# Kernel optimization log

Hardware: AMD Instinct MI355X
Metric: run time of the kernel (lower is better)

The kernel has to match this reference:

```python
import jax, jax.numpy as jnp
import numpy as np
import math

HIDDEN = 2048
N_HEADS = 32
N_KV_HEADS = 8
HEAD_DIM = HIDDEN // N_HEADS  # 64
N_REP = N_HEADS // N_KV_HEADS  # 4
ROPE_THETA = 10000.0
BSZ, SEQ = 2, 2048


def setup_inputs() -> dict:
    key = jax.random.key(0)
    ks = jax.random.split(key, 6)
    hidden_states = jax.random.normal(ks[0], (BSZ, SEQ, HIDDEN), dtype=jnp.float32)
    wq = jax.random.normal(ks[1], (HIDDEN, N_HEADS * HEAD_DIM), dtype=jnp.float32) * (HIDDEN ** -0.5)
    wk = jax.random.normal(ks[2], (HIDDEN, N_KV_HEADS * HEAD_DIM), dtype=jnp.float32) * (HIDDEN ** -0.5)
    wv = jax.random.normal(ks[3], (HIDDEN, N_KV_HEADS * HEAD_DIM), dtype=jnp.float32) * (HIDDEN ** -0.5)
    wo = jax.random.normal(ks[4], (N_HEADS * HEAD_DIM, HIDDEN), dtype=jnp.float32) * (HIDDEN ** -0.5)
    # additive causal mask [b, 1, q, kv]
    neg = jnp.finfo(jnp.float32).min
    causal = jnp.where(jnp.tril(jnp.ones((SEQ, SEQ), dtype=bool)), 0.0, neg)
    attention_mask = jnp.broadcast_to(causal[None, None], (BSZ, 1, SEQ, SEQ)).astype(jnp.float32)
    position_ids = jnp.broadcast_to(jnp.arange(SEQ, dtype=jnp.int32)[None], (BSZ, SEQ))
    return {
        "hidden_states": hidden_states,
        "wq": wq, "wk": wk, "wv": wv, "wo": wo,
        "attention_mask": attention_mask,
        "position_ids": position_ids,
    }


def _rope_cache(seq_len, dtype):
    inv_freq = 1.0 / (ROPE_THETA ** (jnp.arange(0, HEAD_DIM, 2, dtype=jnp.float32) / HEAD_DIM))
    t = jnp.arange(seq_len, dtype=jnp.float32)
    freqs = jnp.outer(t, inv_freq)              # [S, head_dim/2]
    emb = jnp.concatenate([freqs, freqs], -1)   # [S, head_dim]
    return jnp.cos(emb).astype(dtype), jnp.sin(emb).astype(dtype)


def _rotate_half(x):
    x1, x2 = jnp.split(x, 2, axis=-1)
    return jnp.concatenate([-x2, x1], axis=-1)


def reference(hidden_states, wq, wk, wv, wo, attention_mask, position_ids):
    b, s, _ = hidden_states.shape
    q = (hidden_states @ wq).reshape(b, s, N_HEADS, HEAD_DIM).transpose(0, 2, 1, 3)
    k = (hidden_states @ wk).reshape(b, s, N_KV_HEADS, HEAD_DIM).transpose(0, 2, 1, 3)
    v = (hidden_states @ wv).reshape(b, s, N_KV_HEADS, HEAD_DIM).transpose(0, 2, 1, 3)

    cos_c, sin_c = _rope_cache(s, hidden_states.dtype)
    cos = cos_c[position_ids][:, None]  # [b,1,s,head_dim]
    sin = sin_c[position_ids][:, None]
    q = q * cos + _rotate_half(q) * sin
    k = k * cos + _rotate_half(k) * sin

    # repeat_kv: [b, kvh, s, d] -> [b, kvh*n_rep, s, d]
    k = jnp.broadcast_to(k[:, :, None], (b, N_KV_HEADS, N_REP, s, HEAD_DIM)).reshape(b, N_HEADS, s, HEAD_DIM)
    v = jnp.broadcast_to(v[:, :, None], (b, N_KV_HEADS, N_REP, s, HEAD_DIM)).reshape(b, N_HEADS, s, HEAD_DIM)

    scores = jnp.einsum('bhqd,bhkd->bhqk', q, k) / math.sqrt(HEAD_DIM)
    scores = scores + attention_mask
    probs = jax.nn.softmax(scores.astype(jnp.float32), axis=-1).astype(q.dtype)
    attn = jnp.einsum('bhqk,bhkd->bhqd', probs, v)  # [b,h,s,d]
    attn = attn.transpose(0, 2, 1, 3).reshape(b, s, N_HEADS * HEAD_DIM)
    return attn @ wo
```

## Files before the change

kernel.cpp:

```cpp
#include <hip/hip_runtime.h>
#include <math.h>


typedef float f32x4 __attribute__((ext_vector_type(4)));
typedef short s16x8 __attribute__((ext_vector_type(8)));
typedef unsigned short u16x4 __attribute__((ext_vector_type(4)));

__device__ __forceinline__ unsigned short f2bf(float x) {
    union { float f; unsigned int u; } v; v.f = x;
    unsigned int r = v.u + 0x7FFF + ((v.u >> 16) & 1);
    return (unsigned short)(r >> 16);
}

__global__ __launch_bounds__(256) void cast_f32_bf16(
    const float* __restrict__ in, unsigned short* __restrict__ out) {
    size_t i = (size_t)blockIdx.x * 256 + threadIdx.x;
    f32x4 v = *(const f32x4*)&in[i * 4];
    u16x4 r;
    r[0] = f2bf(v[0]); r[1] = f2bf(v[1]); r[2] = f2bf(v[2]); r[3] = f2bf(v[3]);
    *(u16x4*)&out[i * 4] = r;
}

__global__ __launch_bounds__(256) void transpose_cast_all(
    const float* __restrict__ Wq, const float* __restrict__ Wk,
    const float* __restrict__ Wv, const float* __restrict__ Wo,
    unsigned short* __restrict__ Wqkvt, unsigned short* __restrict__ Wot) {
    __shared__ float t[32][33];
    const int bx = blockIdx.x;
    const float* W; unsigned short* Out; int N, n0, nb;
    if (bx < 64)      { W = Wq; Out = Wqkvt; N = 2048; n0 = 0;    nb = bx; }
    else if (bx < 80) { W = Wk; Out = Wqkvt; N = 512;  n0 = 2048; nb = bx - 64; }
    else if (bx < 96) { W = Wv; Out = Wqkvt; N = 512;  n0 = 2560; nb = bx - 80; }
    else              { W = Wo; Out = Wot;   N = 2048; n0 = 0;    nb = bx - 96; }
    int kb = blockIdx.y * 32; nb *= 32;
    int tx = threadIdx.x & 31, ty = threadIdx.x >> 5;
#pragma unroll
    for (int i = 0; i < 4; ++i)
        t[ty + i * 8][tx] = W[(size_t)(kb + ty + i * 8) * N + nb + tx];
    __syncthreads();
#pragma unroll
    for (int i = 0; i < 4; ++i)
        Out[(size_t)(n0 + nb + ty + i * 8) * 2048 + kb + tx] = f2bf(t[tx][ty + i * 8]);
}

__global__ __launch_bounds__(256) void gemm_bf16_nt(
    const unsigned short* __restrict__ A, const unsigned short* __restrict__ Bt,
    float* __restrict__ C, int K, int ldc) {
    __shared__ unsigned short As[128 * 64];
    __shared__ unsigned short Bs[128 * 64];
    const int tid = threadIdx.x;
    const int wave = tid >> 6, lane = tid & 63;
    const int col = lane & 15, quad = lane >> 4;
    const int m0 = blockIdx.y * 128, n0 = blockIdx.x * 128;
    const int wm = (wave >> 1) * 64, wn = (wave & 1) * 64;

    const int lrow = lane >> 3;
    const int gch = (lane & 7) ^ lrow;
    const unsigned short* Ag = A + (size_t)(m0 + wave * 32 + lrow) * K + gch * 8;
    const unsigned short* Bg = Bt + (size_t)(n0 + wave * 32 + lrow) * K + gch * 8;
    unsigned short* AsW = As + wave * 2048;
    unsigned short* BsW = Bs + wave * 2048;

    f32x4 acc[4][4] = {};

    for (int k0 = 0; k0 < K; k0 += 64) {
#pragma unroll
        for (int i = 0; i < 4; ++i) {
            __builtin_amdgcn_global_load_lds(
                (const __attribute__((address_space(1))) void*)(Ag + (size_t)i * 8 * K + k0),
                (__attribute__((address_space(3))) void*)(AsW + i * 512), 16, 0, 0);
            __builtin_amdgcn_global_load_lds(
                (const __attribute__((address_space(1))) void*)(Bg + (size_t)i * 8 * K + k0),
                (__attribute__((address_space(3))) void*)(BsW + i * 512), 16, 0, 0);
        }
        __syncthreads();
#pragma unroll
        for (int ks = 0; ks < 2; ++ks) {
            const int slot = ((ks << 2) + quad) ^ (col & 7);
            s16x8 af[4], bf[4];
#pragma unroll
            for (int mi = 0; mi < 4; ++mi)
                af[mi] = *(const s16x8*)&As[(wm + mi * 16 + col) * 64 + slot * 8];
#pragma unroll
            for (int ni = 0; ni < 4; ++ni)
                bf[ni] = *(const s16x8*)&Bs[(wn + ni * 16 + col) * 64 + slot * 8];
#pragma unroll
            for (int mi = 0; mi < 4; ++mi)
#pragma unroll
                for (int ni = 0; ni < 4; ++ni)
                    acc[mi][ni] = __builtin_amdgcn_mfma_f32_16x16x32_bf16(
                        af[mi], bf[ni], acc[mi][ni], 0, 0, 0);
        }
        __syncthreads();
    }
#pragma unroll
    for (int mi = 0; mi < 4; ++mi)
#pragma unroll
        for (int ni = 0; ni < 4; ++ni)
#pragma unroll
            for (int r = 0; r < 4; ++r) {
                int m = m0 + wm + mi * 16 + quad * 4 + r;
                int n = n0 + wn + ni * 16 + col;
                C[(size_t)m * ldc + n] = acc[mi][ni][r];
            }
}

__global__ __launch_bounds__(256) void rope_pack(
    const float* __restrict__ QKV, const int* __restrict__ pos,
    unsigned short* __restrict__ Qb, unsigned short* __restrict__ Kb,
    unsigned short* __restrict__ Vt) {
    const int bs = blockIdx.x;
    const int b = bs >> 11, s = bs & 2047;
    const int tid = threadIdx.x;
    const float p = (float)pos[bs];
    const float* row = QKV + (size_t)bs * 3072;
    const float NEG_LN_TH_32 = -0.28782313662425575f;

#pragma unroll
    for (int t = 0; t < 4; ++t) {
        int idx = tid + t * 256;
        int hh = idx >> 5, i = idx & 31;
        float inv = __expf((float)i * NEG_LN_TH_32);
        float sn, cs; sincosf(p * inv, &sn, &cs);
        float a = row[hh * 64 + i], bb = row[hh * 64 + i + 32];
        size_t base = ((size_t)(b * 32 + hh) * 2048 + s) * 64;
        Qb[base + i]      = f2bf((a * cs - bb * sn) * 0.125f);
        Qb[base + i + 32] = f2bf((bb * cs + a * sn) * 0.125f);
    }
    {
        int idx = tid;
        int hh = idx >> 5, i = idx & 31;
        float inv = __expf((float)i * NEG_LN_TH_32);
        float sn, cs; sincosf(p * inv, &sn, &cs);
        float a = row[2048 + hh * 64 + i], bb = row[2048 + hh * 64 + i + 32];
        size_t base = ((size_t)(b * 8 + hh) * 2048 + s) * 64;
        Kb[base + i]      = f2bf(a * cs - bb * sn);
        Kb[base + i + 32] = f2bf(bb * cs + a * sn);
    }
#pragma unroll
    for (int t = 0; t < 2; ++t) {
        int idx = tid + t * 256;
        int hh = idx >> 6, d = idx & 63;
        Vt[((size_t)(b * 8 + hh) * 64 + d) * 2048 + s] = f2bf(row[2560 + idx]);
    }
}

__global__ __launch_bounds__(256) void flash_attn(
    const unsigned short* __restrict__ Qb, const unsigned short* __restrict__ Kb,
    const unsigned short* __restrict__ Vt, unsigned short* __restrict__ Ob) {
    __shared__ unsigned short Ks[64 * 64];
    __shared__ unsigned short Vs[64 * 64];
    __shared__ unsigned short Ps[4][32 * 64];

    const int tid = threadIdx.x;
    const int wave = tid >> 6, lane = tid & 63;
    const int col = lane & 15, quad = lane >> 4;

    const int id = blockIdx.x;
    const int rs = id >> 8, u = id & 255;
    const int a = u & 15;
    const int qt = (rs & 1) ? (15 - a) : a;
    const int bh = (u >> 4) + (rs << 4);
    const int q0 = qt * 128;
    const int b = bh >> 5, h = bh & 31, kvh = h >> 2;
    const int qw = q0 + wave * 32;
    const int kv0max = qw & ~63;

    const unsigned short* Qg  = Qb + ((size_t)(b * 32 + h) * 2048) * 64;
    const unsigned short* Kgb = Kb + ((size_t)(b * 8 + kvh) * 2048) * 64;
    const unsigned short* Vgb = Vt + ((size_t)(b * 8 + kvh) * 64) * 2048;

    const int r8 = lane >> 3, g = (lane & 7) ^ r8;
    const unsigned short* KgL = Kgb + (size_t)(wave * 16 + r8) * 64 + g * 8;
    const unsigned short* VgL = Vgb + (size_t)(wave * 16 + r8) * 2048 + g * 8;
    unsigned short* KsW = Ks + wave * 16 * 64;
    unsigned short* VsW = Vs + wave * 16 * 64;

    const s16x8 onesf = {16256, 16256, 16256, 16256, 16256, 16256, 16256, 16256};

    s16x8 qf[2][2];
#pragma unroll
    for (int ni = 0; ni < 2; ++ni)
#pragma unroll
        for (int ks = 0; ks < 2; ++ks)
            qf[ni][ks] = *(const s16x8*)&Qg[(size_t)(qw + ni * 16 + col) * 64 + ks * 32 + quad * 8];

    f32x4 acc_o[2][4] = {};
    f32x4 acc_l[2] = {};

    for (int kv0 = 0; kv0 < q0 + 128; kv0 += 64) {
#pragma unroll
        for (int i = 0; i < 2; ++i) {
            __builtin_amdgcn_global_load_lds(
                (const __attribute__((address_space(1))) void*)(KgL + (size_t)(kv0 + i * 8) * 64),
                (__attribute__((address_space(3))) void*)(KsW + i * 512), 16, 0, 0);
            __builtin_amdgcn_global_load_lds(
                (const __attribute__((address_space(1))) void*)(VgL + kv0 + i * 8 * 2048),
                (__attribute__((address_space(3))) void*)(VsW + i * 512), 16, 0, 0);
        }
        __syncthreads();
        if (kv0 <= kv0max) {
            f32x4 sc[4][2] = {};
#pragma unroll
            for (int ks = 0; ks < 2; ++ks) {
                const int slot = ((ks << 2) + quad) ^ (col & 7);
                s16x8 kf[4];
#pragma unroll
                for (int mi = 0; mi < 4; ++mi)
                    kf[mi] = *(const s16x8*)&Ks[(mi * 16 + col) * 64 + slot * 8];
#pragma unroll
                for (int mi = 0; mi < 4; ++mi)
#pragma unroll
                    for (int ni = 0; ni < 2; ++ni)
                        sc[mi][ni] = __builtin_amdgcn_mfma_f32_16x16x32_bf16(
                            kf[mi], qf[ni][ks], sc[mi][ni], 0, 0, 0);
            }
            if (kv0 == kv0max) {
#pragma unroll
                for (int mi = 0; mi < 4; ++mi)
#pragma unroll
                    for (int ni = 0; ni < 2; ++ni) {
                        int kvb = kv0 + mi * 16 + quad * 4;
                        int q = qw + ni * 16 + col;
#pragma unroll
                        for (int r = 0; r < 4; ++r)
                            if (kvb + r > q) sc[mi][ni][r] = -1e30f;
                    }
            }
#pragma unroll
            for (int mi = 0; mi < 4; ++mi)
#pragma unroll
                for (int ni = 0; ni < 2; ++ni) {
                    unsigned eb[4];
#pragma unroll
                    for (int r = 0; r < 4; ++r)
                        eb[r] = __float_as_uint(__expf(sc[mi][ni][r]));
                    uint2 pk;
                    pk.x = __builtin_amdgcn_perm(eb[1], eb[0], 0x07060302u);
                    pk.y = __builtin_amdgcn_perm(eb[3], eb[2], 0x07060302u);
                    int chl = ((mi * 2 + (quad >> 1)) ^ (col & 7));
                    *(uint2*)&Ps[wave][(ni * 16 + col) * 64 + chl * 8 + (quad & 1) * 4] = pk;
                }
            asm volatile("s_waitcnt lgkmcnt(0)" ::: "memory");
#pragma unroll
            for (int ks = 0; ks < 2; ++ks) {
                const int slot = ((ks << 2) + quad) ^ (col & 7);
                s16x8 pf[2], vf[4];
#pragma unroll
                for (int mi = 0; mi < 2; ++mi)
                    pf[mi] = *(const s16x8*)&Ps[wave][(mi * 16 + col) * 64 + slot * 8];
#pragma unroll
                for (int di = 0; di < 4; ++di)
                    vf[di] = *(const s16x8*)&Vs[(di * 16 + col) * 64 + slot * 8];
#pragma unroll
                for (int mi = 0; mi < 2; ++mi) {
                    acc_l[mi] = __builtin_amdgcn_mfma_f32_16x16x32_bf16(
                        pf[mi], onesf, acc_l[mi], 0, 0, 0);
#pragma unroll
                    for (int di = 0; di < 4; ++di)
                        acc_o[mi][di] = __builtin_amdgcn_mfma_f32_16x16x32_bf16(
                            pf[mi], vf[di], acc_o[mi][di], 0, 0, 0);
                }
            }
        }
        __syncthreads();
    }
#pragma unroll
    for (int mi = 0; mi < 2; ++mi)
#pragma unroll
        for (int r = 0; r < 4; ++r) {
            int qg = qw + mi * 16 + quad * 4 + r;
            float inv = 1.f / acc_l[mi][r];
            size_t base = ((size_t)b * 2048 + qg) * 2048 + h * 64;
#pragma unroll
            for (int di = 0; di < 4; ++di)
                Ob[base + di * 16 + col] = f2bf(acc_o[mi][di][r] * inv);
        }
}

extern "C" void kernel_launch(void* const* d_in, const int* in_sizes, int n_in,
                              void* d_out, int out_size, void* d_ws, size_t ws_size,
                              hipStream_t stream) {
    const float* X  = (const float*)d_in[0];
    const float* Wq = (const float*)d_in[1];
    const float* Wk = (const float*)d_in[2];
    const float* Wv = (const float*)d_in[3];
    const float* Wo = (const float*)d_in[4];
    const int* pos  = (const int*)d_in[6];
    float* out = (float*)d_out;

    char* ws = (char*)d_ws;
    unsigned short* Xb    = (unsigned short*)(ws + 0);
    unsigned short* Wqkvt = (unsigned short*)(ws + 16777216);
    unsigned short* Wot   = (unsigned short*)(ws + 29360128);
    float*          QKVf  = (float*)(ws + 37748736);
    unsigned short* Qb    = (unsigned short*)(ws + 88080384);
    unsigned short* Kb    = (unsigned short*)(ws + 104857600);
    unsigned short* Vt    = (unsigned short*)(ws + 109051904);
    unsigned short* Attn  = Xb;

    cast_f32_bf16<<<8192, 256, 0, stream>>>(X, Xb);
    transpose_cast_all<<<dim3(160, 64), 256, 0, stream>>>(Wq, Wk, Wv, Wo, Wqkvt, Wot);
    gemm_bf16_nt<<<dim3(24, 32), 256, 0, stream>>>(Xb, Wqkvt, QKVf, 2048, 3072);
    rope_pack<<<4096, 256, 0, stream>>>(QKVf, pos, Qb, Kb, Vt);
    flash_attn<<<1024, 256, 0, stream>>>(Qb, Kb, Vt, Attn);
    gemm_bf16_nt<<<dim3(16, 32), 256, 0, stream>>>(Attn, Wot, out, 2048, 2048);
}
```

Baseline: 354.5 us.

## Fuse RoPE into QKV GEMM epilogue and pair causal query tiles in attention

The QKV projection GEMM now applies rotary embedding and the query scale in its epilogue and writes bf16 Q/K/V directly. This removes the fp32 QKV intermediate round trip and the separate rope_pack kernel. A small transpose kernel produces the transposed V layout. Flash attention is restructured so each block handles a mirrored pair of 64-row query tiles (early and late) that share K/V loads, balancing causal work per block, and adds an occupancy hint of 4 in the launch bounds.

```diff
diff --git a/kernel.cpp b/kernel.cpp
--- a/kernel.cpp
+++ b/kernel.cpp
@@ -43,6 +43,104 @@
         Out[(size_t)(n0 + nb + ty + i * 8) * 2048 + kb + tx] = f2bf(t[tx][ty + i * 8]);
 }
 
+__global__ __launch_bounds__(256) void gemm_qkv_rope(
+    const unsigned short* __restrict__ A, const unsigned short* __restrict__ Bt,
+    const int* __restrict__ pos,
+    unsigned short* __restrict__ Qb, unsigned short* __restrict__ Kb,
+    unsigned short* __restrict__ Vb) {
+    const int K = 2048;
+    __shared__ unsigned short As[128 * 64];
+    __shared__ unsigned short Bs[128 * 64];
+    const int tid = threadIdx.x;
+    const int wave = tid >> 6, lane = tid & 63;
+    const int col = lane & 15, quad = lane >> 4;
+    const int m0 = blockIdx.y * 128, n0 = blockIdx.x * 128;
+    const int wm = (wave >> 1) * 64, wn = (wave & 1) * 64;
+
+    const int lrow = lane >> 3;
+    const int gch = (lane & 7) ^ lrow;
+    const unsigned short* Ag = A + (size_t)(m0 + wave * 32 + lrow) * K + gch * 8;
+    const unsigned short* Bg = Bt + (size_t)(n0 + wave * 32 + lrow) * K + gch * 8;
+    unsigned short* AsW = As + wave * 2048;
+    unsigned short* BsW = Bs + wave * 2048;
+
+    f32x4 acc[4][4] = {};
+
+    for (int k0 = 0; k0 < K; k0 += 64) {
+#pragma unroll
+        for (int i = 0; i < 4; ++i) {
+            __builtin_amdgcn_global_load_lds(
+                (const __attribute__((address_space(1))) void*)(Ag + (size_t)i * 8 * K + k0),
+                (__attribute__((address_space(3))) void*)(AsW + i * 512), 16, 0, 0);
+            __builtin_amdgcn_global_load_lds(
+                (const __attribute__((address_space(1))) void*)(Bg + (size_t)i * 8 * K + k0),
+                (__attribute__((address_space(3))) void*)(BsW + i * 512), 16, 0, 0);
+        }
+        __syncthreads();
+#pragma unroll
+        for (int ks = 0; ks < 2; ++ks) {
+            const int slot = ((ks << 2) + quad) ^ (col & 7);
+            s16x8 af[4], bf[4];
+#pragma unroll
+            for (int mi = 0; mi < 4; ++mi)
+                af[mi] = *(const s16x8*)&As[(wm + mi * 16 + col) * 64 + slot * 8];
+#pragma unroll
+            for (int ni = 0; ni < 4; ++ni)
+                bf[ni] = *(const s16x8*)&Bs[(wn + ni * 16 + col) * 64 + slot * 8];
+#pragma unroll
+            for (int mi = 0; mi < 4; ++mi)
+#pragma unroll
+                for (int ni = 0; ni < 4; ++ni)
+                    acc[mi][ni] = __builtin_amdgcn_mfma_f32_16x16x32_bf16(
+                        af[mi], bf[ni], acc[mi][ni], 0, 0, 0);
+        }
+        __syncthreads();
+    }
+
+    const int cb = n0 + wn;
+    if (cb >= 2560) {
+        const int hd = (cb - 2560) >> 6;
+#pragma unroll
+        for (int mi = 0; mi < 4; ++mi)
+#pragma unroll
+            for (int r = 0; r < 4; ++r) {
+                int m = m0 + wm + mi * 16 + quad * 4 + r;
+                int b = m >> 11, s = m & 2047;
+                size_t rb = ((size_t)(b * 8 + hd) * 2048 + s) * 64;
+#pragma unroll
+                for (int ni = 0; ni < 4; ++ni)
+                    Vb[rb + ni * 16 + col] = f2bf(acc[mi][ni][r]);
+            }
+    } else {
+        const int isQ = (cb < 2048);
+        const int hd = isQ ? (cb >> 6) : ((cb - 2048) >> 6);
+        const int nh = isQ ? 32 : 8;
+        const float scale = isQ ? 0.125f : 1.0f;
+        unsigned short* Out = isQ ? Qb : Kb;
+        const float NEG_LN_TH_32 = -0.28782313662425575f;
+        const float inv0 = __expf((float)col * NEG_LN_TH_32);
+        const float inv1 = __expf((float)(col + 16) * NEG_LN_TH_32);
+#pragma unroll
+        for (int mi = 0; mi < 4; ++mi)
+#pragma unroll
+            for (int r = 0; r < 4; ++r) {
+                int m = m0 + wm + mi * 16 + quad * 4 + r;
+                int b = m >> 11, s = m & 2047;
+                float p = (float)pos[m];
+                float sn0, cs0, sn1, cs1;
+                __sincosf(p * inv0, &sn0, &cs0);
+                __sincosf(p * inv1, &sn1, &cs1);
+                float a0 = acc[mi][0][r], a1 = acc[mi][1][r];
+                float b0 = acc[mi][2][r], b1 = acc[mi][3][r];
+                size_t rb = ((size_t)(b * nh + hd) * 2048 + s) * 64;
+                Out[rb + col]      = f2bf((a0 * cs0 - b0 * sn0) * scale);
+                Out[rb + col + 16] = f2bf((a1 * cs1 - b1 * sn1) * scale);
+                Out[rb + col + 32] = f2bf((b0 * cs0 + a0 * sn0) * scale);
+                Out[rb + col + 48] = f2bf((b1 * cs1 + a1 * sn1) * scale);
+            }
+    }
+}
+
 __global__ __launch_bounds__(256) void gemm_bf16_nt(
     const unsigned short* __restrict__ A, const unsigned short* __restrict__ Bt,
     float* __restrict__ C, int K, int ldc) {
@@ -105,66 +203,46 @@
             }
 }
 
-__global__ __launch_bounds__(256) void rope_pack(
-    const float* __restrict__ QKV, const int* __restrict__ pos,
-    unsigned short* __restrict__ Qb, unsigned short* __restrict__ Kb,
-    unsigned short* __restrict__ Vt) {
-    const int bs = blockIdx.x;
-    const int b = bs >> 11, s = bs & 2047;
-    const int tid = threadIdx.x;
-    const float p = (float)pos[bs];
-    const float* row = QKV + (size_t)bs * 3072;
-    const float NEG_LN_TH_32 = -0.28782313662425575f;
-
-#pragma unroll
-    for (int t = 0; t < 4; ++t) {
-        int idx = tid + t * 256;
-        int hh = idx >> 5, i = idx & 31;
-        float inv = __expf((float)i * NEG_LN_TH_32);
-        float sn, cs; sincosf(p * inv, &sn, &cs);
-        float a = row[hh * 64 + i], bb = row[hh * 64 + i + 32];
-        size_t base = ((size_t)(b * 32 + hh) * 2048 + s) * 64;
-        Qb[base + i]      = f2bf((a * cs - bb * sn) * 0.125f);
-        Qb[base + i + 32] = f2bf((bb * cs + a * sn) * 0.125f);
-    }
-    {
-        int idx = tid;
-        int hh = idx >> 5, i = idx & 31;
-        float inv = __expf((float)i * NEG_LN_TH_32);
-        float sn, cs; sincosf(p * inv, &sn, &cs);
-        float a = row[2048 + hh * 64 + i], bb = row[2048 + hh * 64 + i + 32];
-        size_t base = ((size_t)(b * 8 + hh) * 2048 + s) * 64;
-        Kb[base + i]      = f2bf(a * cs - bb * sn);
-        Kb[base + i + 32] = f2bf(bb * cs + a * sn);
-    }
-#pragma unroll
-    for (int t = 0; t < 2; ++t) {
-        int idx = tid + t * 256;
-        int hh = idx >> 6, d = idx & 63;
-        Vt[((size_t)(b * 8 + hh) * 64 + d) * 2048 + s] = f2bf(row[2560 + idx]);
-    }
-}
-
-__global__ __launch_bounds__(256) void flash_attn(
+__global__ __launch_bounds__(256) void transpose_v(
+    const unsigned short* __restrict__ Vb, unsigned short* __restrict__ Vt) {
+    __shared__ unsigned short t[64 * 66];
+    const int bh = blockIdx.x >> 5, st = blockIdx.x & 31;
+    const unsigned short* src = Vb + ((size_t)bh * 2048 + st * 64) * 64;
+    unsigned short* dst = Vt + (size_t)bh * 64 * 2048 + st * 64;
+    const int r = threadIdx.x >> 2, c = (threadIdx.x & 3) * 16;
+    s16x8 v0 = *(const s16x8*)&src[r * 64 + c];
+    s16x8 v1 = *(const s16x8*)&src[r * 64 + c + 8];
+    unsigned* tw = (unsigned*)&t[r * 66 + c];
+#pragma unroll
+    for (int q2 = 0; q2 < 4; ++q2) tw[q2] = ((unsigned*)&v0)[q2];
+#pragma unroll
+    for (int q2 = 0; q2 < 4; ++q2) tw[4 + q2] = ((unsigned*)&v1)[q2];
+    __syncthreads();
+    const int d = threadIdx.x >> 2, sc2 = (threadIdx.x & 3) * 16;
+    unsigned short outv[16];
+#pragma unroll
+    for (int jj = 0; jj < 16; ++jj) outv[jj] = t[(sc2 + jj) * 66 + d];
+    *(s16x8*)&dst[(size_t)d * 2048 + sc2] = *(s16x8*)&outv[0];
+    *(s16x8*)&dst[(size_t)d * 2048 + sc2 + 8] = *(s16x8*)&outv[8];
+}
+
+__global__ __launch_bounds__(256, 4) void flash_attn(
     const unsigned short* __restrict__ Qb, const unsigned short* __restrict__ Kb,
     const unsigned short* __restrict__ Vt, unsigned short* __restrict__ Ob) {
     __shared__ unsigned short Ks[64 * 64];
     __shared__ unsigned short Vs[64 * 64];
-    __shared__ unsigned short Ps[4][32 * 64];
+    __shared__ unsigned short PsA[4][16 * 64];
+    __shared__ unsigned short PsB[4][16 * 64];
 
     const int tid = threadIdx.x;
     const int wave = tid >> 6, lane = tid & 63;
     const int col = lane & 15, quad = lane >> 4;
 
     const int id = blockIdx.x;
-    const int rs = id >> 8, u = id & 255;
-    const int a = u & 15;
-    const int qt = (rs & 1) ? (15 - a) : a;
-    const int bh = (u >> 4) + (rs << 4);
-    const int q0 = qt * 128;
+    const int j = id & 15, bh = id >> 4;
     const int b = bh >> 5, h = bh & 31, kvh = h >> 2;
-    const int qw = q0 + wave * 32;
-    const int kv0max = qw & ~63;
+    const int qA0 = (31 - j) * 64, qB0 = j * 64;
+    const int qwA = qA0 + wave * 16, qwB = qB0 + wave * 16;
 
     const unsigned short* Qg  = Qb + ((size_t)(b * 32 + h) * 2048) * 64;
     const unsigned short* Kgb = Kb + ((size_t)(b * 8 + kvh) * 2048) * 64;
@@ -178,104 +256,120 @@
 
     const s16x8 onesf = {16256, 16256, 16256, 16256, 16256, 16256, 16256, 16256};
 
-    s16x8 qf[2][2];
-#pragma unroll
-    for (int ni = 0; ni < 2; ++ni)
-#pragma unroll
-        for (int ks = 0; ks < 2; ++ks)
-            qf[ni][ks] = *(const s16x8*)&Qg[(size_t)(qw + ni * 16 + col) * 64 + ks * 32 + quad * 8];
-
-    f32x4 acc_o[2][4] = {};
-    f32x4 acc_l[2] = {};
-
-    for (int kv0 = 0; kv0 < q0 + 128; kv0 += 64) {
-#pragma unroll
-        for (int i = 0; i < 2; ++i) {
-            __builtin_amdgcn_global_load_lds(
-                (const __attribute__((address_space(1))) void*)(KgL + (size_t)(kv0 + i * 8) * 64),
-                (__attribute__((address_space(3))) void*)(KsW + i * 512), 16, 0, 0);
-            __builtin_amdgcn_global_load_lds(
-                (const __attribute__((address_space(1))) void*)(VgL + kv0 + i * 8 * 2048),
-                (__attribute__((address_space(3))) void*)(VsW + i * 512), 16, 0, 0);
-        }
-        __syncthreads();
-        if (kv0 <= kv0max) {
-            f32x4 sc[4][2] = {};
-#pragma unroll
-            for (int ks = 0; ks < 2; ++ks) {
-                const int slot = ((ks << 2) + quad) ^ (col & 7);
-                s16x8 kf[4];
-#pragma unroll
-                for (int mi = 0; mi < 4; ++mi)
-                    kf[mi] = *(const s16x8*)&Ks[(mi * 16 + col) * 64 + slot * 8];
-#pragma unroll
-                for (int mi = 0; mi < 4; ++mi)
-#pragma unroll
-                    for (int ni = 0; ni < 2; ++ni)
-                        sc[mi][ni] = __builtin_amdgcn_mfma_f32_16x16x32_bf16(
-                            kf[mi], qf[ni][ks], sc[mi][ni], 0, 0, 0);
-            }
-            if (kv0 == kv0max) {
-#pragma unroll
-                for (int mi = 0; mi < 4; ++mi)
-#pragma unroll
-                    for (int ni = 0; ni < 2; ++ni) {
-                        int kvb = kv0 + mi * 16 + quad * 4;
-                        int q = qw + ni * 16 + col;
-#pragma unroll
-                        for (int r = 0; r < 4; ++r)
-                            if (kvb + r > q) sc[mi][ni][r] = -1e30f;
-                    }
-            }
-#pragma unroll
-            for (int mi = 0; mi < 4; ++mi)
-#pragma unroll
-                for (int ni = 0; ni < 2; ++ni) {
-                    unsigned eb[4];
+    s16x8 qfA[2], qfB[2];
+#pragma unroll
+    for (int ks = 0; ks < 2; ++ks) {
+        qfA[ks] = *(const s16x8*)&Qg[(size_t)(qwA + col) * 64 + ks * 32 + quad * 8];
+        qfB[ks] = *(const s16x8*)&Qg[(size_t)(qwB + col) * 64 + ks * 32 + quad * 8];
+    }
+
+    f32x4 aoA[4] = {}, aoB[4] = {};
+    f32x4 alA = {}, alB = {};
+
+    for (int kv0 = 0; kv0 <= qA0; kv0 += 64) {
+        __builtin_amdgcn_global_load_lds(
+            (const __attribute__((address_space(1))) void*)(KgL + (size_t)kv0 * 64),
+            (__attribute__((address_space(3))) void*)KsW, 16, 0, 0);
+        __builtin_amdgcn_global_load_lds(
+            (const __attribute__((address_space(1))) void*)(KgL + (size_t)kv0 * 64 + 512),
+            (__attribute__((address_space(3))) void*)(KsW + 512), 16, 0, 0);
+        __builtin_amdgcn_global_load_lds(
+            (const __attribute__((address_space(1))) void*)(VgL + kv0),
+            (__attribute__((address_space(3))) void*)VsW, 16, 0, 0);
+        __builtin_amdgcn_global_load_lds(
+            (const __attribute__((address_space(1))) void*)(VgL + kv0 + 8 * 2048),
+            (__attribute__((address_space(3))) void*)(VsW + 512), 16, 0, 0);
+        __syncthreads();
+
+        const bool doB = (kv0 <= qB0);
+#pragma unroll
+        for (int mi = 0; mi < 4; ++mi) {
+            const int s0 = (quad) ^ (col & 7);
+            const int s1 = (4 + quad) ^ (col & 7);
+            s16x8 kf0 = *(const s16x8*)&Ks[(mi * 16 + col) * 64 + s0 * 8];
+            s16x8 kf1 = *(const s16x8*)&Ks[(mi * 16 + col) * 64 + s1 * 8];
+            {
+                f32x4 sc = {};
+                sc = __builtin_amdgcn_mfma_f32_16x16x32_bf16(kf0, qfA[0], sc, 0, 0, 0);
+                sc = __builtin_amdgcn_mfma_f32_16x16x32_bf16(kf1, qfA[1], sc, 0, 0, 0);
+                if (kv0 == qA0) {
+                    int kvb = kv0 + mi * 16 + quad * 4, q = qwA + col;
 #pragma unroll
                     for (int r = 0; r < 4; ++r)
-                        eb[r] = __float_as_uint(__expf(sc[mi][ni][r]));
-                    uint2 pk;
-                    pk.x = __builtin_amdgcn_perm(eb[1], eb[0], 0x07060302u);
-                    pk.y = __builtin_amdgcn_perm(eb[3], eb[2], 0x07060302u);
-                    int chl = ((mi * 2 + (quad >> 1)) ^ (col & 7));
-                    *(uint2*)&Ps[wave][(ni * 16 + col) * 64 + chl * 8 + (quad & 1) * 4] = pk;
+                        if (kvb + r > q) sc[r] = -1e30f;
                 }
-            asm volatile("s_waitcnt lgkmcnt(0)" ::: "memory");
-#pragma unroll
-            for (int ks = 0; ks < 2; ++ks) {
-                const int slot = ((ks << 2) + quad) ^ (col & 7);
-                s16x8 pf[2], vf[4];
-#pragma unroll
-                for (int mi = 0; mi < 2; ++mi)
-                    pf[mi] = *(const s16x8*)&Ps[wave][(mi * 16 + col) * 64 + slot * 8];
+                unsigned eb[4];
+#pragma unroll
+                for (int r = 0; r < 4; ++r) eb[r] = __float_as_uint(__expf(sc[r]));
+                uint2 pk;
+                pk.x = __builtin_amdgcn_perm(eb[1], eb[0], 0x07060302u);
+                pk.y = __builtin_amdgcn_perm(eb[3], eb[2], 0x07060302u);
+                int chl = (mi * 2 + (quad >> 1)) ^ (col & 7);
+                *(uint2*)&PsA[wave][col * 64 + chl * 8 + (quad & 1) * 4] = pk;
+            }
+            if (doB) {
+                f32x4 sc = {};
+                sc = __builtin_amdgcn_mfma_f32_16x16x32_bf16(kf0, qfB[0], sc, 0, 0, 0);
+                sc = __builtin_amdgcn_mfma_f32_16x16x32_bf16(kf1, qfB[1], sc, 0, 0, 0);
+                if (kv0 == qB0) {
+                    int kvb = kv0 + mi * 16 + quad * 4, q = qwB + col;
+#pragma unroll
+                    for (int r = 0; r < 4; ++r)
+                        if (kvb + r > q) sc[r] = -1e30f;
+                }
+                unsigned eb[4];
+#pragma unroll
+                for (int r = 0; r < 4; ++r) eb[r] = __float_as_uint(__expf(sc[r]));
+                uint2 pk;
+                pk.x = __builtin_amdgcn_perm(eb[1], eb[0], 0x07060302u);
+                pk.y = __builtin_amdgcn_perm(eb[3], eb[2], 0x07060302u);
+                int chl = (mi * 2 + (quad >> 1)) ^ (col & 7);
+                *(uint2*)&PsB[wave][col * 64 + chl * 8 + (quad & 1) * 4] = pk;
+            }
+        }
+        asm volatile("s_waitcnt lgkmcnt(0)" ::: "memory");
+#pragma unroll
+        for (int ks = 0; ks < 2; ++ks) {
+            const int slot = ((ks << 2) + quad) ^ (col & 7);
+            s16x8 vf[4];
+#pragma unroll
+            for (int di = 0; di < 4; ++di)
+                vf[di] = *(const s16x8*)&Vs[(di * 16 + col) * 64 + slot * 8];
+            s16x8 pfA = *(const s16x8*)&PsA[wave][col * 64 + slot * 8];
+            alA = __builtin_amdgcn_mfma_f32_16x16x32_bf16(pfA, onesf, alA, 0, 0, 0);
+#pragma unroll
+            for (int di = 0; di < 4; ++di)
+                aoA[di] = __builtin_amdgcn_mfma_f32_16x16x32_bf16(pfA, vf[di], aoA[di], 0, 0, 0);
+            if (doB) {
+                s16x8 pfB = *(const s16x8*)&PsB[wave][col * 64 + slot * 8];
+                alB = __builtin_amdgcn_mfma_f32_16x16x32_bf16(pfB, onesf, alB, 0, 0, 0);
 #pragma unroll
                 for (int di = 0; di < 4; ++di)
-                    vf[di] = *(const s16x8*)&Vs[(di * 16 + col) * 64 + slot * 8];
-#pragma unroll
-                for (int mi = 0; mi < 2; ++mi) {
-                    acc_l[mi] = __builtin_amdgcn_mfma_f32_16x16x32_bf16(
-                        pf[mi], onesf, acc_l[mi], 0, 0, 0);
-#pragma unroll
-                    for (int di = 0; di < 4; ++di)
-                        acc_o[mi][di] = __builtin_amdgcn_mfma_f32_16x16x32_bf16(
-                            pf[mi], vf[di], acc_o[mi][di], 0, 0, 0);
-                }
-            }
-        }
-        __syncthreads();
-    }
-#pragma unroll
-    for (int mi = 0; mi < 2; ++mi)
-#pragma unroll
-        for (int r = 0; r < 4; ++r) {
-            int qg = qw + mi * 16 + quad * 4 + r;
-            float inv = 1.f / acc_l[mi][r];
+                    aoB[di] = __builtin_amdgcn_mfma_f32_16x16x32_bf16(pfB, vf[di], aoB[di], 0, 0, 0);
+            }
+        }
+        __syncthreads();
+    }
+
+#pragma unroll
+    for (int r = 0; r < 4; ++r) {
+        {
+            int qg = qwA + quad * 4 + r;
+            float inv = 1.f / alA[r];
             size_t base = ((size_t)b * 2048 + qg) * 2048 + h * 64;
 #pragma unroll
             for (int di = 0; di < 4; ++di)
-                Ob[base + di * 16 + col] = f2bf(acc_o[mi][di][r] * inv);
-        }
+                Ob[base + di * 16 + col] = f2bf(aoA[di][r] * inv);
+        }
+        {
+            int qg = qwB + quad * 4 + r;
+            float inv = 1.f / alB[r];
+            size_t base = ((size_t)b * 2048 + qg) * 2048 + h * 64;
+#pragma unroll
+            for (int di = 0; di < 4; ++di)
+                Ob[base + di * 16 + col] = f2bf(aoB[di][r] * inv);
+        }
+    }
 }
 
 extern "C" void kernel_launch(void* const* d_in, const int* in_sizes, int n_in,
@@ -293,16 +387,16 @@
     unsigned short* Xb    = (unsigned short*)(ws + 0);
     unsigned short* Wqkvt = (unsigned short*)(ws + 16777216);
     unsigned short* Wot   = (unsigned short*)(ws + 29360128);
-    float*          QKVf  = (float*)(ws + 37748736);
-    unsigned short* Qb    = (unsigned short*)(ws + 88080384);
-    unsigned short* Kb    = (unsigned short*)(ws + 104857600);
-    unsigned short* Vt    = (unsigned short*)(ws + 109051904);
+    unsigned short* Qb    = (unsigned short*)(ws + 37748736);
+    unsigned short* Kb    = (unsigned short*)(ws + 54525952);
+    unsigned short* Vb    = (unsigned short*)(ws + 58720256);
+    unsigned short* Vt    = (unsigned short*)(ws + 62914560);
     unsigned short* Attn  = Xb;
 
     cast_f32_bf16<<<8192, 256, 0, stream>>>(X, Xb);
     transpose_cast_all<<<dim3(160, 64), 256, 0, stream>>>(Wq, Wk, Wv, Wo, Wqkvt, Wot);
-    gemm_bf16_nt<<<dim3(24, 32), 256, 0, stream>>>(Xb, Wqkvt, QKVf, 2048, 3072);
-    rope_pack<<<4096, 256, 0, stream>>>(QKVf, pos, Qb, Kb, Vt);
+    gemm_qkv_rope<<<dim3(24, 32), 256, 0, stream>>>(Xb, Wqkvt, pos, Qb, Kb, Vb);
+    transpose_v<<<512, 256, 0, stream>>>(Vb, Vt);
     flash_attn<<<1024, 256, 0, stream>>>(Qb, Kb, Vt, Attn);
     gemm_bf16_nt<<<dim3(16, 32), 256, 0, stream>>>(Attn, Wot, out, 2048, 2048);
 }
```

After: 316.9 us. 1.12x faster.
